# Optimization experiments

Hardware: AMD Instinct MI355X
Metric: run time of the kernel (lower is better)

The kernel has to match this reference:

```python
import jax, jax.numpy as jnp
import numpy as np

N = 8192
D_IN = 128
D_OUT = 128

def setup_inputs() -> dict:
    key = jax.random.key(0)
    k_x, k_q, k_k, k_v = jax.random.split(key, 4)
    scale = 1.0 / np.sqrt(D_IN)
    return {
        "input": jax.random.normal(k_x, (N, D_IN), dtype=jnp.float32),
        # torch Linear weights: [out_features, in_features]
        "Wq": jax.random.normal(k_q, (D_IN, D_IN), dtype=jnp.float32) * scale,
        "Wk": jax.random.normal(k_k, (D_IN, D_IN), dtype=jnp.float32) * scale,
        "Wv": jax.random.normal(k_v, (D_OUT, D_IN), dtype=jnp.float32) * scale,
    }

def reference(input, Wq, Wk, Wv):
    # torch Linear: y = x @ W.T
    Q = input @ Wq.T          # [N, d_in]
    K = input @ Wk.T          # [N, d_in]
    V = input @ Wv.T          # [N, d_out]
    # NOTE: original module has NO 1/sqrt(d) scaling — keep it faithful.
    W = jax.nn.softmax(Q @ K.T, axis=-1)  # [N, N]
    return W @ V              # [N, d_out]
```

## Files before the change

kernel.cpp:

```cpp
#include <hip/hip_runtime.h>
#include <hip/hip_bf16.h>
#include <stdint.h>

#define N_TOK 8192
#define D 128
#define QTILES (N_TOK / 16)
#define KVB 64
#define KVTILES (N_TOK / KVB)
#define LOG2E 1.4426950408889634f

typedef __attribute__((ext_vector_type(8))) short short8;
typedef __attribute__((ext_vector_type(4))) short short4v;
typedef __attribute__((ext_vector_type(4))) float f32x4;
typedef __attribute__((ext_vector_type(8))) _Float16 half8;
typedef __attribute__((ext_vector_type(4))) _Float16 half4;
typedef __attribute__((ext_vector_type(2))) __fp16 fp16x2;

__device__ __forceinline__ ushort f2bf(float f) {
    union { float f; uint32_t u; } cv; cv.f = f;
    uint32_t u = cv.u;
    return (ushort)((u + 0x7fffu + ((u >> 16) & 1u)) >> 16);
}
__device__ __forceinline__ float bf2f(ushort h) {
    union { uint32_t u; float f; } cv; cv.u = ((uint32_t)h) << 16;
    return cv.f;
}
__device__ __forceinline__ f32x4 zero4() {
    f32x4 z; z[0] = 0.f; z[1] = 0.f; z[2] = 0.f; z[3] = 0.f; return z;
}
__device__ __forceinline__ float ex2(float x) {
    return __builtin_amdgcn_exp2f(x);
}
__device__ __forceinline__ float max16(const f32x4* s) {
    float a = fmaxf(fmaxf(s[0][0], s[0][1]), s[0][2]);
    float b = fmaxf(fmaxf(s[0][3], s[1][0]), s[1][1]);
    float c = fmaxf(fmaxf(s[1][2], s[1][3]), s[2][0]);
    float d = fmaxf(fmaxf(s[2][1], s[2][2]), s[2][3]);
    float e = fmaxf(fmaxf(s[3][0], s[3][1]), s[3][2]);
    return fmaxf(fmaxf(fmaxf(a, b), c), fmaxf(fmaxf(d, e), s[3][3]));
}

__global__ void cvt_kernel(const float* __restrict__ Wq, const float* __restrict__ Wk,
                           const float* __restrict__ Wv,
                           ushort* __restrict__ Whi, ushort* __restrict__ Wlo) {
    int i = blockIdx.x * blockDim.x + threadIdx.x;
    int w = i * 4;
    if (w >= 3 * 16384) return;
    int m = w >> 14;
    int off = w & 16383;
    const float* src = (m == 0) ? Wq : ((m == 1) ? Wk : Wv);
    ushort* dhi = Whi + (m << 14);
    ushort* dlo = Wlo + (m << 14);
    f32x4 v = *(const f32x4*)(src + off);
    short4v ph, pl;
    #pragma unroll
    for (int r = 0; r < 4; ++r) {
        ushort h = f2bf(v[r]);
        ph[r] = (short)h;
        pl[r] = (short)f2bf(v[r] - bf2f(h));
    }
    *(short4v*)(dhi + off) = ph;
    *(short4v*)(dlo + off) = pl;
}

__global__ __launch_bounds__(256) void proj_kernel(
    const float* __restrict__ X,
    const ushort* __restrict__ Whi, const ushort* __restrict__ Wlo,
    ushort* __restrict__ Qh, ushort* __restrict__ Kh, ushort* __restrict__ Vt) {
    const int tid = threadIdx.x;
    const int lane = tid & 63;
    const int wid = tid >> 6;
    const int g = lane >> 4, r16 = lane & 15;
    const int qbase = blockIdx.x * 32;

    short8 xh[2][4], xl[2][4];
    #pragma unroll
    for (int qa = 0; qa < 2; ++qa) {
        const float* xr = X + (size_t)(qbase + 16 * qa + r16) * D + 8 * g;
        #pragma unroll
        for (int ds = 0; ds < 4; ++ds) {
            f32x4 a = *(const f32x4*)(xr + 32 * ds);
            f32x4 b = *(const f32x4*)(xr + 32 * ds + 4);
            #pragma unroll
            for (int j = 0; j < 4; ++j) {
                ushort h = f2bf(a[j]);
                xh[qa][ds][j] = (short)h;
                xl[qa][ds][j] = (short)f2bf(a[j] - bf2f(h));
                ushort h2 = f2bf(b[j]);
                xh[qa][ds][4 + j] = (short)h2;
                xl[qa][ds][4 + j] = (short)f2bf(b[j] - bf2f(h2));
            }
        }
    }

    #pragma unroll
    for (int m = 0; m < 2; ++m) {
        const ushort* Wh = Whi + m * 16384;
        const ushort* Wl = Wlo + m * 16384;
        ushort* O = m ? Kh : Qh;
        const float sc = m ? 1.0f : LOG2E;
        #pragma unroll
        for (int jj = 0; jj < 2; ++jj) {
            int jt = 2 * wid + jj;
            const ushort* wrh = Wh + (size_t)(16 * jt + r16) * D + 8 * g;
            const ushort* wrl = Wl + (size_t)(16 * jt + r16) * D + 8 * g;
            f32x4 acc[2] = {zero4(), zero4()};
            #pragma unroll
            for (int ds = 0; ds < 4; ++ds) {
                short8 wh = *(const short8*)(wrh + 32 * ds);
                short8 wl = *(const short8*)(wrl + 32 * ds);
                #pragma unroll
                for (int qa = 0; qa < 2; ++qa) {
                    acc[qa] = __builtin_amdgcn_mfma_f32_16x16x32_bf16(wh, xh[qa][ds], acc[qa], 0, 0, 0);
                    acc[qa] = __builtin_amdgcn_mfma_f32_16x16x32_bf16(wh, xl[qa][ds], acc[qa], 0, 0, 0);
                    acc[qa] = __builtin_amdgcn_mfma_f32_16x16x32_bf16(wl, xh[qa][ds], acc[qa], 0, 0, 0);
                }
            }
            #pragma unroll
            for (int qa = 0; qa < 2; ++qa) {
                half4 pk;
                #pragma unroll
                for (int r = 0; r < 4; ++r) pk[r] = (_Float16)(acc[qa][r] * sc);
                *(half4*)(O + (size_t)(qbase + 16 * qa + r16) * D + 16 * jt + 4 * g) = pk;
            }
        }
    }
    {
        const ushort* Wh = Whi + 32768;
        const ushort* Wl = Wlo + 32768;
        #pragma unroll
        for (int jj = 0; jj < 2; ++jj) {
            int jt = 2 * wid + jj;
            const ushort* wrh = Wh + (size_t)(16 * jt + r16) * D + 8 * g;
            const ushort* wrl = Wl + (size_t)(16 * jt + r16) * D + 8 * g;
            f32x4 acc[2] = {zero4(), zero4()};
            #pragma unroll
            for (int ds = 0; ds < 4; ++ds) {
                short8 wh = *(const short8*)(wrh + 32 * ds);
                short8 wl = *(const short8*)(wrl + 32 * ds);
                #pragma unroll
                for (int qa = 0; qa < 2; ++qa) {
                    acc[qa] = __builtin_amdgcn_mfma_f32_16x16x32_bf16(xh[qa][ds], wh, acc[qa], 0, 0, 0);
                    acc[qa] = __builtin_amdgcn_mfma_f32_16x16x32_bf16(xl[qa][ds], wh, acc[qa], 0, 0, 0);
                    acc[qa] = __builtin_amdgcn_mfma_f32_16x16x32_bf16(xh[qa][ds], wl, acc[qa], 0, 0, 0);
                }
            }
            #pragma unroll
            for (int qa = 0; qa < 2; ++qa) {
                half4 pk;
                #pragma unroll
                for (int r = 0; r < 4; ++r) pk[r] = (_Float16)acc[qa][r];
                *(half4*)(Vt + (size_t)(16 * jt + r16) * N_TOK + qbase + 16 * qa + 4 * g) = pk;
            }
        }
    }
}

template<int NS>
__global__ __launch_bounds__(256, 2) void flash_kernel(
    const ushort* __restrict__ Qh, const ushort* __restrict__ Kh,
    const ushort* __restrict__ Vt, ushort* __restrict__ Opb, float* __restrict__ ML) {
    __shared__ __align__(16) ushort K_lds[2][KVB * D];
    __shared__ __align__(16) ushort V_lds[2][D * KVB];
    __shared__ __align__(16) ushort P_lds[4 * 2048];

    const int tid = threadIdx.x;
    const int lane = tid & 63;
    const int wid = tid >> 6;
    const int g = lane >> 4, r16 = lane & 15;
    const int sp = blockIdx.x % NS;
    const int qg = blockIdx.x / NS;
    const int t0 = (KVTILES * sp) / NS;
    const int t1 = (KVTILES * (sp + 1)) / NS;
    const int qbase = qg * 128 + wid * 32;
    const int pswz = (r16 & 7) << 3;

    half8 qf[2][4];
    #pragma unroll
    for (int qa = 0; qa < 2; ++qa) {
        const ushort* qr = Qh + (size_t)(qbase + 16 * qa + r16) * D + 8 * g;
        #pragma unroll
        for (int ds = 0; ds < 4; ++ds)
            qf[qa][ds] = *(const half8*)(qr + 32 * ds);
    }

    float m[2] = {-INFINITY, -INFINITY}, l[2] = {0.f, 0.f};
    f32x4 o[2][8];
    #pragma unroll
    for (int qa = 0; qa < 2; ++qa)
        #pragma unroll
        for (int dt = 0; dt < 8; ++dt) o[qa][dt] = zero4();

    ushort* P_w = &P_lds[wid * 2048];

    short8 sk[4], sv[4];

    auto LOADT = [&](int it) {
        const int kv = it * KVB;
        #pragma unroll
        for (int rr = 0; rr < 4; ++rr) {
            int idx = tid + 256 * rr;
            int row = idx >> 4, seg = idx & 15;
            sk[rr] = *(const short8*)(Kh + (size_t)(kv + row) * D + seg * 8);
        }
        #pragma unroll
        for (int rr = 0; rr < 4; ++rr) {
            int idx = tid + 256 * rr;
            int row = idx >> 3, seg = idx & 7;
            sv[rr] = *(const short8*)(Vt + (size_t)row * N_TOK + kv + seg * 8);
        }
    };
    auto WRITET = [&](int b) {
        #pragma unroll
        for (int rr = 0; rr < 4; ++rr) {
            int idx = tid + 256 * rr;
            int row = idx >> 4, seg = idx & 15;
            *(short8*)&K_lds[b][(row * 128 + seg * 8) ^ ((row & 7) << 3)] = sk[rr];
        }
        #pragma unroll
        for (int rr = 0; rr < 4; ++rr) {
            int idx = tid + 256 * rr;
            int row = idx >> 3, seg = idx & 7;
            *(short8*)&V_lds[b][(row * 64 + seg * 8) ^ ((row & 7) << 3)] = sv[rr];
        }
    };

    LOADT(t0);
    WRITET(0);
    __syncthreads();

    int buf = 0;
    for (int it = t0; it < t1; ++it) {
        if (it + 1 < t1) LOADT(it + 1);

        const ushort* kb = K_lds[buf];
        const ushort* vb = V_lds[buf];

        f32x4 s[2][4];
        #pragma unroll
        for (int qa = 0; qa < 2; ++qa)
            #pragma unroll
            for (int t = 0; t < 4; ++t) s[qa][t] = zero4();
        __builtin_amdgcn_s_setprio(1);
        #pragma unroll
        for (int t = 0; t < 4; ++t) {
            #pragma unroll
            for (int ds = 0; ds < 4; ++ds) {
                int row = 16 * t + r16;
                half8 kf = *(const half8*)&kb[(row * 128 + 32 * ds + 8 * g) ^ ((row & 7) << 3)];
                #pragma unroll
                for (int qa = 0; qa < 2; ++qa)
                    s[qa][t] = __builtin_amdgcn_mfma_f32_16x16x32_f16(kf, qf[qa][ds], s[qa][t], 0, 0, 0);
            }
        }
        __builtin_amdgcn_s_setprio(0);

        #pragma unroll
        for (int qa = 0; qa < 2; ++qa) {
            float tm = max16(s[qa]);
            tm = fmaxf(tm, __shfl_xor(tm, 16));
            tm = fmaxf(tm, __shfl_xor(tm, 32));
            if (!__all(tm <= m[qa])) {
                float mnew = fmaxf(m[qa], tm);
                float scale = ex2(m[qa] - mnew);
                l[qa] *= scale;
                #pragma unroll
                for (int dt = 0; dt < 8; ++dt) o[qa][dt] *= scale;
                m[qa] = mnew;
            }
            float psum = 0.f;
            #pragma unroll
            for (int t = 0; t < 4; ++t) {
                float p0 = ex2(s[qa][t][0] - m[qa]);
                float p1 = ex2(s[qa][t][1] - m[qa]);
                float p2 = ex2(s[qa][t][2] - m[qa]);
                float p3 = ex2(s[qa][t][3] - m[qa]);
                psum += (p0 + p1) + (p2 + p3);
                union { fp16x2 h[2]; short4v s4; } u;
                u.h[0] = __builtin_amdgcn_cvt_pkrtz(p0, p1);
                u.h[1] = __builtin_amdgcn_cvt_pkrtz(p2, p3);
                *(short4v*)&P_w[(qa * 1024 + r16 * 64 + 16 * t + 4 * g) ^ pswz] = u.s4;
            }
            psum += __shfl_xor(psum, 16);
            psum += __shfl_xor(psum, 32);
            l[qa] += psum;
        }

        __builtin_amdgcn_s_setprio(1);
        #pragma unroll
        for (int c = 0; c < 2; ++c) {
            half8 pf0 = *(const half8*)&P_w[(r16 * 64 + 32 * c + 8 * g) ^ pswz];
            half8 pf1 = *(const half8*)&P_w[(1024 + r16 * 64 + 32 * c + 8 * g) ^ pswz];
            #pragma unroll
            for (int dt = 0; dt < 8; ++dt) {
                int row = 16 * dt + r16;
                half8 vf = *(const half8*)&vb[(row * 64 + 32 * c + 8 * g) ^ ((row & 7) << 3)];
                o[0][dt] = __builtin_amdgcn_mfma_f32_16x16x32_f16(vf, pf0, o[0][dt], 0, 0, 0);
                o[1][dt] = __builtin_amdgcn_mfma_f32_16x16x32_f16(vf, pf1, o[1][dt], 0, 0, 0);
            }
        }
        __builtin_amdgcn_s_setprio(0);

        if (it + 1 < t1) WRITET(buf ^ 1);
        __syncthreads();
        buf ^= 1;
    }

    #pragma unroll
    for (int qa = 0; qa < 2; ++qa) {
        ushort* obase = Opb + ((size_t)sp * N_TOK + qbase + 16 * qa + r16) * D + 4 * g;
        #pragma unroll
        for (int dt = 0; dt < 8; ++dt) {
            half4 pk;
            #pragma unroll
            for (int r = 0; r < 4; ++r) pk[r] = (_Float16)o[qa][dt][r];
            *(half4*)(obase + 16 * dt) = pk;
        }
        if (g == 0) {
            int qt = (qbase + 16 * qa) >> 4;
            float* ml = ML + ((size_t)sp * QTILES + qt) * 32;
            ml[r16] = m[qa];
            ml[16 + r16] = l[qa];
        }
    }
}

template<int NS>
__global__ void merge_kernel(const ushort* __restrict__ Opb, const float* __restrict__ ML,
                             float* __restrict__ out) {
    int i = blockIdx.x * blockDim.x + threadIdx.x;
    int e = i * 4;
    if (e >= N_TOK * D) return;
    int q = e >> 7;
    int qt = q >> 4, qr = q & 15;
    float mv[NS], lv[NS];
    float M = -INFINITY;
    #pragma unroll
    for (int s = 0; s < NS; ++s) {
        const float* ml = ML + ((size_t)s * QTILES + qt) * 32;
        mv[s] = ml[qr];
        lv[s] = ml[16 + qr];
        M = fmaxf(M, mv[s]);
    }
    float L = 0.f, a[NS];
    #pragma unroll
    for (int s = 0; s < NS; ++s) { a[s] = __builtin_amdgcn_exp2f(mv[s] - M); L += a[s] * lv[s]; }
    float inv = 1.f / L;
    f32x4 acc = zero4();
    #pragma unroll
    for (int s = 0; s < NS; ++s) {
        half4 ov = *(const half4*)(Opb + (size_t)s * N_TOK * D + e);
        #pragma unroll
        for (int r = 0; r < 4; ++r) acc[r] += (float)ov[r] * a[s];
    }
    *(f32x4*)(out + e) = acc * inv;
}

extern "C" void kernel_launch(void* const* d_in, const int* in_sizes, int n_in,
                              void* d_out, int out_size, void* d_ws, size_t ws_size,
                              hipStream_t stream) {
    const float* X  = (const float*)d_in[0];
    const float* Wq = (const float*)d_in[1];
    const float* Wk = (const float*)d_in[2];
    const float* Wv = (const float*)d_in[3];
    float* out = (float*)d_out;

    char* ws = (char*)d_ws;
    ushort* Whi = (ushort*)(ws);
    ushort* Wlo = (ushort*)(ws + 98304);
    ushort* Qh  = (ushort*)(ws + 196608);
    ushort* Kh  = (ushort*)(ws + 2293760);
    ushort* Vt  = (ushort*)(ws + 4390912);
    ushort* Opb = (ushort*)(ws + 6488064);

    const size_t op_off = 6488064;
    const size_t need8 = op_off + (size_t)8 * N_TOK * D * 2 + (size_t)8 * QTILES * 32 * 4;

    cvt_kernel<<<48, 256, 0, stream>>>(Wq, Wk, Wv, Whi, Wlo);
    proj_kernel<<<256, 256, 0, stream>>>(X, Whi, Wlo, Qh, Kh, Vt);

    if (ws_size >= need8) {
        float* ML = (float*)(ws + op_off + (size_t)8 * N_TOK * D * 2);
        flash_kernel<8><<<(N_TOK / 128) * 8, 256, 0, stream>>>(Qh, Kh, Vt, Opb, ML);
        merge_kernel<8><<<(N_TOK * D / 4 + 255) / 256, 256, 0, stream>>>(Opb, ML, out);
    } else {
        float* ML = (float*)(ws + op_off + (size_t)4 * N_TOK * D * 2);
        flash_kernel<4><<<(N_TOK / 128) * 4, 256, 0, stream>>>(Qh, Kh, Vt, Opb, ML);
        merge_kernel<4><<<(N_TOK * D / 4 + 255) / 256, 256, 0, stream>>>(Opb, ML, out);
    }
}
```

Measured before the change: 76.18 us.

## Use 512-thread flash blocks with single-buffered shared K/V and 16-way KV split

Each flash-attention block now has 8 waves covering 256 queries, so every K/V tile staged in LDS is reused by twice as many queries and global K/V traffic per query is halved. LDS double buffering is replaced by a single buffer with an extra barrier before the next tile is written. When the workspace is large enough, the launcher also uses a 16-way KV split. The tighter launch bounds (512, 4) may force register spills of the large accumulator state, and the added barrier exposes load latency that double buffering used to hide.

Result: slower. 243.5 us (+219.7%).

```diff
diff --git a/kernel.cpp b/kernel.cpp
--- a/kernel.cpp
+++ b/kernel.cpp
@@ -157,12 +157,12 @@
 }
 
 template<int NS>
-__global__ __launch_bounds__(256, 2) void flash_kernel(
+__global__ __launch_bounds__(512, 4) void flash_kernel(
     const ushort* __restrict__ Qh, const ushort* __restrict__ Kh,
     const ushort* __restrict__ Vt, ushort* __restrict__ Opb, float* __restrict__ ML) {
-    __shared__ __align__(16) ushort K_lds[2][KVB * D];
-    __shared__ __align__(16) ushort V_lds[2][D * KVB];
-    __shared__ __align__(16) ushort P_lds[4 * 2048];
+    __shared__ __align__(16) ushort K_lds[KVB * D];
+    __shared__ __align__(16) ushort V_lds[D * KVB];
+    __shared__ __align__(16) ushort P_lds[8 * 2048];
 
     const int tid = threadIdx.x;
     const int lane = tid & 63;
@@ -172,7 +172,7 @@
     const int qg = blockIdx.x / NS;
     const int t0 = (KVTILES * sp) / NS;
     const int t1 = (KVTILES * (sp + 1)) / NS;
-    const int qbase = qg * 128 + wid * 32;
+    const int qbase = qg * 256 + wid * 32;
     const int pswz = (r16 & 7) << 3;
 
     half8 qf[2][4];
@@ -193,49 +193,45 @@
 
     ushort* P_w = &P_lds[wid * 2048];
 
-    short8 sk[4], sv[4];
+    short8 sk[2], sv[2];
 
     auto LOADT = [&](int it) {
         const int kv = it * KVB;
         #pragma unroll
-        for (int rr = 0; rr < 4; ++rr) {
-            int idx = tid + 256 * rr;
+        for (int rr = 0; rr < 2; ++rr) {
+            int idx = tid + 512 * rr;
             int row = idx >> 4, seg = idx & 15;
             sk[rr] = *(const short8*)(Kh + (size_t)(kv + row) * D + seg * 8);
         }
         #pragma unroll
-        for (int rr = 0; rr < 4; ++rr) {
-            int idx = tid + 256 * rr;
+        for (int rr = 0; rr < 2; ++rr) {
+            int idx = tid + 512 * rr;
             int row = idx >> 3, seg = idx & 7;
             sv[rr] = *(const short8*)(Vt + (size_t)row * N_TOK + kv + seg * 8);
         }
     };
-    auto WRITET = [&](int b) {
-        #pragma unroll
-        for (int rr = 0; rr < 4; ++rr) {
-            int idx = tid + 256 * rr;
+    auto WRITET = [&]() {
+        #pragma unroll
+        for (int rr = 0; rr < 2; ++rr) {
+            int idx = tid + 512 * rr;
             int row = idx >> 4, seg = idx & 15;
-            *(short8*)&K_lds[b][(row * 128 + seg * 8) ^ ((row & 7) << 3)] = sk[rr];
-        }
-        #pragma unroll
-        for (int rr = 0; rr < 4; ++rr) {
-            int idx = tid + 256 * rr;
+            *(short8*)&K_lds[(row * 128 + seg * 8) ^ ((row & 7) << 3)] = sk[rr];
+        }
+        #pragma unroll
+        for (int rr = 0; rr < 2; ++rr) {
+            int idx = tid + 512 * rr;
             int row = idx >> 3, seg = idx & 7;
-            *(short8*)&V_lds[b][(row * 64 + seg * 8) ^ ((row & 7) << 3)] = sv[rr];
+            *(short8*)&V_lds[(row * 64 + seg * 8) ^ ((row & 7) << 3)] = sv[rr];
         }
     };
 
     LOADT(t0);
-    WRITET(0);
+    WRITET();
     __syncthreads();
 
-    int buf = 0;
     for (int it = t0; it < t1; ++it) {
         if (it + 1 < t1) LOADT(it + 1);
 
-        const ushort* kb = K_lds[buf];
-        const ushort* vb = V_lds[buf];
-
         f32x4 s[2][4];
         #pragma unroll
         for (int qa = 0; qa < 2; ++qa)
@@ -247,7 +243,7 @@
             #pragma unroll
             for (int ds = 0; ds < 4; ++ds) {
                 int row = 16 * t + r16;
-                half8 kf = *(const half8*)&kb[(row * 128 + 32 * ds + 8 * g) ^ ((row & 7) << 3)];
+                half8 kf = *(const half8*)&K_lds[(row * 128 + 32 * ds + 8 * g) ^ ((row & 7) << 3)];
                 #pragma unroll
                 for (int qa = 0; qa < 2; ++qa)
                     s[qa][t] = __builtin_amdgcn_mfma_f32_16x16x32_f16(kf, qf[qa][ds], s[qa][t], 0, 0, 0);
@@ -294,16 +290,16 @@
             #pragma unroll
             for (int dt = 0; dt < 8; ++dt) {
                 int row = 16 * dt + r16;
-                half8 vf = *(const half8*)&vb[(row * 64 + 32 * c + 8 * g) ^ ((row & 7) << 3)];
+                half8 vf = *(const half8*)&V_lds[(row * 64 + 32 * c + 8 * g) ^ ((row & 7) << 3)];
                 o[0][dt] = __builtin_amdgcn_mfma_f32_16x16x32_f16(vf, pf0, o[0][dt], 0, 0, 0);
                 o[1][dt] = __builtin_amdgcn_mfma_f32_16x16x32_f16(vf, pf1, o[1][dt], 0, 0, 0);
             }
         }
         __builtin_amdgcn_s_setprio(0);
 
-        if (it + 1 < t1) WRITET(buf ^ 1);
         __syncthreads();
-        buf ^= 1;
+        if (it + 1 < t1) WRITET();
+        __syncthreads();
     }
 
     #pragma unroll
@@ -374,18 +370,23 @@
     ushort* Opb = (ushort*)(ws + 6488064);
 
     const size_t op_off = 6488064;
-    const size_t need8 = op_off + (size_t)8 * N_TOK * D * 2 + (size_t)8 * QTILES * 32 * 4;
+    const size_t need16 = op_off + (size_t)16 * N_TOK * D * 2 + (size_t)16 * QTILES * 32 * 4;
+    const size_t need8  = op_off + (size_t)8  * N_TOK * D * 2 + (size_t)8  * QTILES * 32 * 4;
 
     cvt_kernel<<<48, 256, 0, stream>>>(Wq, Wk, Wv, Whi, Wlo);
     proj_kernel<<<256, 256, 0, stream>>>(X, Whi, Wlo, Qh, Kh, Vt);
 
-    if (ws_size >= need8) {
+    if (ws_size >= need16) {
+        float* ML = (float*)(ws + op_off + (size_t)16 * N_TOK * D * 2);
+        flash_kernel<16><<<(N_TOK / 256) * 16, 512, 0, stream>>>(Qh, Kh, Vt, Opb, ML);
+        merge_kernel<16><<<(N_TOK * D / 4 + 255) / 256, 256, 0, stream>>>(Opb, ML, out);
+    } else if (ws_size >= need8) {
         float* ML = (float*)(ws + op_off + (size_t)8 * N_TOK * D * 2);
-        flash_kernel<8><<<(N_TOK / 128) * 8, 256, 0, stream>>>(Qh, Kh, Vt, Opb, ML);
+        flash_kernel<8><<<(N_TOK / 256) * 8, 512, 0, stream>>>(Qh, Kh, Vt, Opb, ML);
         merge_kernel<8><<<(N_TOK * D / 4 + 255) / 256, 256, 0, stream>>>(Opb, ML, out);
     } else {
         float* ML = (float*)(ws + op_off + (size_t)4 * N_TOK * D * 2);
-        flash_kernel<4><<<(N_TOK / 128) * 4, 256, 0, stream>>>(Qh, Kh, Vt, Opb, ML);
+        flash_kernel<4><<<(N_TOK / 256) * 4, 512, 0, stream>>>(Qh, Kh, Vt, Opb, ML);
         merge_kernel<4><<<(N_TOK * D / 4 + 255) / 256, 256, 0, stream>>>(Opb, ML, out);
     }
 }
```

## Load V fragments directly from global into registers, drop V LDS staging

Applied to the files above, without the earlier changes.

Removes the shared-memory double buffer for V. Each wave now loads its V MFMA fragments straight from global memory into registers at the start of every KV tile, and launch bounds drop to one block per SIMD pair to make room for the extra registers. The goal is to cut LDS write/read traffic and LDS footprint for V. In exchange, the four waves of a block each fetch the same V tile redundantly from global/L2. V loads are also no longer prefetched a tile ahead, so their latency must hide behind the QK^T and softmax phase, and occupancy may fall.

After: 116.1 us. 52.4% more time.

```diff
diff --git a/kernel.cpp b/kernel.cpp
--- a/kernel.cpp
+++ b/kernel.cpp
@@ -157,11 +157,10 @@
 }
 
 template<int NS>
-__global__ __launch_bounds__(256, 2) void flash_kernel(
+__global__ __launch_bounds__(256, 1) void flash_kernel(
     const ushort* __restrict__ Qh, const ushort* __restrict__ Kh,
     const ushort* __restrict__ Vt, ushort* __restrict__ Opb, float* __restrict__ ML) {
     __shared__ __align__(16) ushort K_lds[2][KVB * D];
-    __shared__ __align__(16) ushort V_lds[2][D * KVB];
     __shared__ __align__(16) ushort P_lds[4 * 2048];
 
     const int tid = threadIdx.x;
@@ -193,9 +192,10 @@
 
     ushort* P_w = &P_lds[wid * 2048];
 
-    short8 sk[4], sv[4];
-
-    auto LOADT = [&](int it) {
+    short8 sk[4];
+    half8 vf[2][8];
+
+    auto LOADK = [&](int it) {
         const int kv = it * KVB;
         #pragma unroll
         for (int rr = 0; rr < 4; ++rr) {
@@ -203,38 +203,34 @@
             int row = idx >> 4, seg = idx & 15;
             sk[rr] = *(const short8*)(Kh + (size_t)(kv + row) * D + seg * 8);
         }
-        #pragma unroll
-        for (int rr = 0; rr < 4; ++rr) {
-            int idx = tid + 256 * rr;
-            int row = idx >> 3, seg = idx & 7;
-            sv[rr] = *(const short8*)(Vt + (size_t)row * N_TOK + kv + seg * 8);
-        }
     };
-    auto WRITET = [&](int b) {
+    auto LOADV = [&](int it) {
+        const int kv = it * KVB;
+        #pragma unroll
+        for (int c = 0; c < 2; ++c)
+            #pragma unroll
+            for (int dt = 0; dt < 8; ++dt)
+                vf[c][dt] = *(const half8*)(Vt + (size_t)(16 * dt + r16) * N_TOK + kv + 32 * c + 8 * g);
+    };
+    auto WRITEK = [&](int b) {
         #pragma unroll
         for (int rr = 0; rr < 4; ++rr) {
             int idx = tid + 256 * rr;
             int row = idx >> 4, seg = idx & 15;
             *(short8*)&K_lds[b][(row * 128 + seg * 8) ^ ((row & 7) << 3)] = sk[rr];
         }
-        #pragma unroll
-        for (int rr = 0; rr < 4; ++rr) {
-            int idx = tid + 256 * rr;
-            int row = idx >> 3, seg = idx & 7;
-            *(short8*)&V_lds[b][(row * 64 + seg * 8) ^ ((row & 7) << 3)] = sv[rr];
-        }
     };
 
-    LOADT(t0);
-    WRITET(0);
+    LOADK(t0);
+    WRITEK(0);
     __syncthreads();
 
     int buf = 0;
     for (int it = t0; it < t1; ++it) {
-        if (it + 1 < t1) LOADT(it + 1);
+        LOADV(it);
+        if (it + 1 < t1) LOADK(it + 1);
 
         const ushort* kb = K_lds[buf];
-        const ushort* vb = V_lds[buf];
 
         f32x4 s[2][4];
         #pragma unroll
@@ -293,15 +289,13 @@
             half8 pf1 = *(const half8*)&P_w[(1024 + r16 * 64 + 32 * c + 8 * g) ^ pswz];
             #pragma unroll
             for (int dt = 0; dt < 8; ++dt) {
-                int row = 16 * dt + r16;
-                half8 vf = *(const half8*)&vb[(row * 64 + 32 * c + 8 * g) ^ ((row & 7) << 3)];
-                o[0][dt] = __builtin_amdgcn_mfma_f32_16x16x32_f16(vf, pf0, o[0][dt], 0, 0, 0);
-                o[1][dt] = __builtin_amdgcn_mfma_f32_16x16x32_f16(vf, pf1, o[1][dt], 0, 0, 0);
+                o[0][dt] = __builtin_amdgcn_mfma_f32_16x16x32_f16(vf[c][dt], pf0, o[0][dt], 0, 0, 0);
+                o[1][dt] = __builtin_amdgcn_mfma_f32_16x16x32_f16(vf[c][dt], pf1, o[1][dt], 0, 0, 0);
             }
         }
         __builtin_amdgcn_s_setprio(0);
 
-        if (it + 1 < t1) WRITET(buf ^ 1);
+        if (it + 1 < t1) WRITEK(buf ^ 1);
         __syncthreads();
         buf ^= 1;
     }
```
